# Kernel tuning notes

Hardware: AMD Instinct MI355X
Metric: run time of the kernel (lower is better)

The kernel has to match this reference:

```python
import jax, jax.numpy as jnp
import numpy as np

B, C, CI, H, W = 4, 256, 128, 64, 64  # batch, in_channels, inter_channels, spatial
EPS = 1e-5


def conv1x1(x, w, b):
    # x: [b,c,h,w], w: [o,c], b: [o] -> [b,o,h,w]
    return jnp.einsum('bchw,oc->bohw', x, w) + b[None, :, None, None]


def setup_inputs() -> dict:
    key = jax.random.key(0)
    ks = jax.random.split(key, 16)
    s_in = 1.0 / np.sqrt(C)
    s_mid = 1.0 / np.sqrt(CI)
    inp = {
        'feats_all': jax.random.normal(ks[0], (B, C, H, W), dtype=jnp.float32),
        'human_feats': jax.random.normal(ks[1], (B, C, H, W), dtype=jnp.float32),
        'g_w': jax.random.uniform(ks[2], (CI, C), jnp.float32, -s_in, s_in),
        'g_b': jax.random.uniform(ks[3], (CI,), jnp.float32, -s_in, s_in),
        'theta_w': jax.random.uniform(ks[4], (CI, C), jnp.float32, -s_in, s_in),
        'theta_b': jax.random.uniform(ks[5], (CI,), jnp.float32, -s_in, s_in),
        'phi_w': jax.random.uniform(ks[6], (CI, C), jnp.float32, -s_in, s_in),
        'phi_b': jax.random.uniform(ks[7], (CI,), jnp.float32, -s_in, s_in),
        'human_theta_w': jax.random.uniform(ks[8], (CI, C), jnp.float32, -s_in, s_in),
        'human_theta_b': jax.random.uniform(ks[9], (CI,), jnp.float32, -s_in, s_in),
        'human_phi_w': jax.random.uniform(ks[10], (CI, C), jnp.float32, -s_in, s_in),
        'human_phi_b': jax.random.uniform(ks[11], (CI,), jnp.float32, -s_in, s_in),
        'W_w': jax.random.uniform(ks[12], (C, CI), jnp.float32, -s_mid, s_mid),
        'W_b': jax.random.uniform(ks[13], (C,), jnp.float32, -s_mid, s_mid),
        'bn_gamma': jax.random.normal(ks[14], (C,), dtype=jnp.float32) * 0.1 + 1.0,
        'bn_beta': jax.random.normal(ks[15], (C,), dtype=jnp.float32) * 0.1,
        'bn_mean': jnp.zeros((C,), jnp.float32),
        'bn_var': jnp.ones((C,), jnp.float32),
    }
    return inp


def reference(feats_all, human_feats, g_w, g_b, theta_w, theta_b, phi_w, phi_b,
              human_theta_w, human_theta_b, human_phi_w, human_phi_b,
              W_w, W_b, bn_gamma, bn_beta, bn_mean, bn_var):
    b = feats_all.shape[0]
    n = H * W
    scale = CI ** -0.5

    # human attention map: softmax over keys of scaled QK^T
    hq = conv1x1(human_feats, human_theta_w, human_theta_b).reshape(b, CI, n)  # [b,ci,n]
    hk = conv1x1(human_feats, human_phi_w, human_phi_b).reshape(b, CI, n)
    human_map = jax.nn.softmax(scale * jnp.einsum('bcq,bck->bqk', hq, hk), axis=-1)

    # standard non-local map on feats_all
    th = conv1x1(feats_all, theta_w, theta_b).reshape(b, CI, n)
    ph = conv1x1(feats_all, phi_w, phi_b).reshape(b, CI, n)
    f = jax.nn.softmax(scale * jnp.einsum('bcq,bck->bqk', th, ph), axis=-1)

    g_x = conv1x1(feats_all, g_w, g_b).reshape(b, CI, n)  # [b,ci,n]

    attn = (human_map + f) * 0.5                          # [b,n,n]
    y = jnp.einsum('bqk,bck->bcq', attn, g_x)             # [b,ci,n]
    y = y.reshape(b, CI, H, W)

    wy = conv1x1(y, W_w, W_b)                             # [b,C,H,W]
    # BatchNorm2d (eval mode, running stats)
    inv = bn_gamma / jnp.sqrt(bn_var + EPS)
    out = (wy - bn_mean[None, :, None, None]) * inv[None, :, None, None] + bn_beta[None, :, None, None]
    return out
```

## Files before the change

### kernel.cpp

```cpp
#include <hip/hip_runtime.h>

#define DEVI __device__ __forceinline__

typedef float f32x4 __attribute__((ext_vector_type(4)));
typedef float f32x16 __attribute__((ext_vector_type(16)));
typedef unsigned int u32x4 __attribute__((ext_vector_type(4)));
typedef unsigned int u32x2 __attribute__((ext_vector_type(2)));
typedef __bf16 bf16x8 __attribute__((ext_vector_type(8)));

#define NB 4
#define CIN 256
#define CI_ 128
#define NN 4096
#define QSCALE 0.12752792233895158f

typedef unsigned short us;

DEVI us f2bf(float f) {
  unsigned int x = __float_as_uint(f);
  x += 0x7FFFu + ((x >> 16) & 1u);
  return (us)(x >> 16);
}

DEVI unsigned cvtpk(float lo, float hi) {
  unsigned r;
  asm("v_cvt_pk_bf16_f32 %0, %1, %2" : "=v"(r) : "v"(lo), "v"(hi));
  return r;
}

DEVI void plswap(unsigned& a, unsigned& b) {
  asm volatile("v_permlane32_swap_b32 %0, %1" : "+v"(a), "+v"(b));
}

DEVI float exp2fast(float x) {
#if __has_builtin(__builtin_amdgcn_exp2f)
  return __builtin_amdgcn_exp2f(x);
#else
  return exp2f(x);
#endif
}

DEVI f32x4 mfma16(u32x4 a, u32x4 b, f32x4 c) {
  return __builtin_amdgcn_mfma_f32_16x16x32_bf16(
      __builtin_bit_cast(bf16x8, a), __builtin_bit_cast(bf16x8, b), c, 0, 0, 0);
}

DEVI f32x16 mfma32(u32x4 a, u32x4 b, f32x16 c) {
  return __builtin_amdgcn_mfma_f32_32x32x16_bf16(
      __builtin_bit_cast(bf16x8, a), __builtin_bit_cast(bf16x8, b), c, 0, 0, 0);
}

DEVI void gload16(const void* g, void* l) {
  __builtin_amdgcn_global_load_lds(
      (const __attribute__((address_space(1))) void*)g,
      (__attribute__((address_space(3))) void*)l, 16, 0, 0);
}

DEVI void softpack(f32x16& a, float& ls, u32x4* pa) {
#pragma unroll
  for (int r = 0; r < 16; ++r) {
    float e = exp2fast(a[r]);
    ls += e;
    a[r] = e;
  }
  unsigned x0 = cvtpk(a[0], a[1]), z0 = cvtpk(a[2], a[3]);
  unsigned y0 = cvtpk(a[4], a[5]), t0 = cvtpk(a[6], a[7]);
  plswap(x0, y0);
  plswap(z0, t0);
  pa[0][0] = x0; pa[0][1] = z0; pa[0][2] = y0; pa[0][3] = t0;
  unsigned x1 = cvtpk(a[8], a[9]), z1 = cvtpk(a[10], a[11]);
  unsigned y1 = cvtpk(a[12], a[13]), t1 = cvtpk(a[14], a[15]);
  plswap(x1, y1);
  plswap(z1, t1);
  pa[1][0] = x1; pa[1][1] = z1; pa[1][2] = y1; pa[1][3] = t1;
}

__global__ __launch_bounds__(256) void wcvt_kernel(
    const float* __restrict__ hth_w, const float* __restrict__ hph_w,
    const float* __restrict__ th_w, const float* __restrict__ ph_w,
    const float* __restrict__ g_w, const float* __restrict__ Ww,
    us* __restrict__ wb) {
  const float* srcs[6] = {hth_w, hph_w, th_w, ph_w, g_w, Ww};
  const float* s = srcs[blockIdx.y];
  us* d = wb + blockIdx.y * 32768;
  int idx = (blockIdx.x * 256 + threadIdx.x) * 4;
  f32x4 v = *(const f32x4*)(s + idx);
  u32x2 o;
  o[0] = cvtpk(v[0], v[1]);
  o[1] = cvtpk(v[2], v[3]);
  *(u32x2*)(d + idx) = o;
}

__global__ __launch_bounds__(256) void proj_kernel(
    const float* __restrict__ feats, const float* __restrict__ human,
    const float* __restrict__ g_b, const float* __restrict__ th_b,
    const float* __restrict__ ph_b, const float* __restrict__ hth_b,
    const float* __restrict__ hph_b, const us* __restrict__ wb,
    us* __restrict__ hqT, us* __restrict__ hkT,
    us* __restrict__ thT, us* __restrict__ phT, us* __restrict__ gP) {
  __shared__ alignas(16) us xt[64 * 256];
  const int t = threadIdx.x;
  const int b = blockIdx.y;
  const int n0 = blockIdx.x * 64;
  const int grp = blockIdx.z;
  const int w = t >> 6, l = t & 63, g16 = l >> 4, l15 = l & 15;
  const int tg = t >> 4, tl = t & 15;

  const float* src = grp ? feats : human;
#pragma unroll
  for (int i = 0; i < 8; ++i) {
    int p = i * 16 + tg;
    const float* s0 = src + (size_t)(b * CIN + 2 * p) * NN + n0 + tl * 4;
    f32x4 v0 = *(const f32x4*)s0;
    f32x4 v1 = *(const f32x4*)(s0 + NN);
#pragma unroll
    for (int j = 0; j < 4; ++j) {
      int row = tl * 4 + j;
      *(unsigned*)((char*)xt + row * 512 + ((4 * p) ^ ((row & 15) << 4))) =
          cvtpk(v0[j], v1[j]);
    }
  }
  __syncthreads();

  const float* pb2[2] = {grp ? th_b : hth_b, grp ? ph_b : hph_b};
  us* pout2[2] = {grp ? thT : hqT, grp ? phT : hkT};
  const us* wb0 = wb + grp * 2 * 32768;

  u32x4 afrag[8];
  const int arow = w * 16 + l15;
#pragma unroll
  for (int s = 0; s < 8; ++s)
    afrag[s] = *(const u32x4*)((const char*)xt + arow * 512 +
                               (((s << 6) | (g16 << 4)) ^ (l15 << 4)));
  for (int p = 0; p < 2; ++p) {
    const us* wbp = wb0 + p * 32768;
    const float scl = (p == 0) ? QSCALE : 1.0f;
    for (int nt = 0; nt < 8; ++nt) {
      f32x4 acc = {0.f, 0.f, 0.f, 0.f};
#pragma unroll
      for (int s = 0; s < 8; ++s) {
        u32x4 bf = *(const u32x4*)(wbp + (nt * 16 + l15) * 256 + s * 32 + g16 * 8);
        acc = mfma16(afrag[s], bf, acc);
      }
      float bias = pb2[p][nt * 16 + l15];
#pragma unroll
      for (int r = 0; r < 4; ++r) {
        int nrow = n0 + w * 16 + g16 * 4 + r;
        pout2[p][((size_t)b * NN + nrow) * CI_ + nt * 16 + l15] =
            f2bf((acc[r] + bias) * scl);
      }
    }
  }

  if (grp) {
    const us* wbg = wb + 4 * 32768;
    u32x4 ag[2][8];
#pragma unroll
    for (int mt = 0; mt < 2; ++mt)
#pragma unroll
      for (int s = 0; s < 8; ++s)
        ag[mt][s] = *(const u32x4*)(wbg + (w * 32 + mt * 16 + l15) * 256 + s * 32 + g16 * 8);
    float gb[2][4];
#pragma unroll
    for (int mt = 0; mt < 2; ++mt)
#pragma unroll
      for (int r = 0; r < 4; ++r) gb[mt][r] = g_b[w * 32 + mt * 16 + g16 * 4 + r];
    for (int nt = 0; nt < 4; ++nt) {
      f32x4 acc0 = {0.f, 0.f, 0.f, 0.f}, acc1 = {0.f, 0.f, 0.f, 0.f};
#pragma unroll
      for (int s = 0; s < 8; ++s) {
        u32x4 bf = *(const u32x4*)((const char*)xt + (nt * 16 + l15) * 512 +
                                   ((s * 64 + g16 * 16) ^ (l15 << 4)));
        acc0 = mfma16(ag[0][s], bf, acc0);
        acc1 = mfma16(ag[1][s], bf, acc1);
      }
#pragma unroll
      for (int r = 0; r < 4; ++r) {
        int ci0 = w * 32 + g16 * 4 + r;
        gP[((size_t)b * CI_ + ci0) * NN + n0 + nt * 16 + l15] = f2bf(acc0[r] + gb[0][r]);
        gP[((size_t)b * CI_ + ci0 + 16) * NN + n0 + nt * 16 + l15] = f2bf(acc1[r] + gb[1][r]);
      }
    }
  }
}

__global__ __launch_bounds__(128, 2) void attn_kernel(
    const us* __restrict__ hqT, const us* __restrict__ hkT,
    const us* __restrict__ thT, const us* __restrict__ phT,
    const us* __restrict__ gP, us* __restrict__ PY, float* __restrict__ PL) {
  __shared__ alignas(16) us sK[2][32 * 128];
  __shared__ alignas(16) us sV[2][32 * 128];

  const int t = threadIdx.x, w = t >> 6, l = t & 63;
  const int l31 = l & 31, hi = l >> 5, l15 = l & 15;
  const int id = blockIdx.x;
  const int bp = id & 7, b = bp & 3, path = bp >> 2;
  const int r2 = id >> 3, h = r2 & 1, chunk = r2 >> 1;
  const int qw = chunk * 64 + w * 32, kb = h * 2048;
  const us* Qs = (path ? thT : hqT) + (size_t)b * NN * CI_;
  const char* Kb = (const char*)((path ? phT : hkT) + (size_t)b * NN * CI_);
  const char* Vb = (const char*)(gP + (size_t)b * CI_ * NN);

  u32x4 aQ[8];
#pragma unroll
  for (int s = 0; s < 8; ++s)
    aQ[s] = *(const u32x4*)(Qs + (size_t)(qw + l31) * CI_ + s * 16 + hi * 8);

  f32x16 Y[4];
#pragma unroll
  for (int ds = 0; ds < 4; ++ds) Y[ds] = 0.f;
  float lsum = 0.f;

  const int sr = l >> 4;

  auto stage = [&](int k0, int buf) {
#pragma unroll
    for (int i = 0; i < 4; ++i) {
      int row = w * 16 + i * 4 + sr;
      gload16(Kb + (size_t)(k0 + row) * 256 + (((l & 15) ^ (row & 15)) << 4),
              (char*)sK[buf] + (w * 16 + i * 4) * 256);
    }
#pragma unroll
    for (int i = 0; i < 4; ++i) {
      int R = w * 16 + i * 4 + sr;
      int lu = (l & 15) ^ (R & 15);
      int d = 4 * R + (lu >> 2);
      gload16(Vb + (size_t)d * 8192 + (size_t)k0 * 2 + (lu & 3) * 16,
              (char*)sV[buf] + (w * 16 + i * 4) * 256);
    }
  };

  stage(kb, 0);
  __syncthreads();

  for (int kt = 0; kt < 64; ++kt) {
    const int cur = kt & 1;
    if (kt < 63) stage(kb + (kt + 1) * 32, cur ^ 1);
    const char* kt_ = (const char*)sK[cur];
    const char* vt_ = (const char*)sV[cur];

    f32x16 a0 = 0.f;
    __builtin_amdgcn_s_setprio(1);
#pragma unroll
    for (int s = 0; s < 8; ++s) {
      u32x4 ak = *(const u32x4*)(kt_ + l31 * 256 + (((s * 2 + hi) ^ l15) << 4));
      a0 = mfma32(ak, aQ[s], a0);
    }
    __builtin_amdgcn_s_setprio(0);

    u32x4 pa[2];
    softpack(a0, lsum, pa);

    __builtin_amdgcn_s_setprio(1);
#pragma unroll
    for (int ds = 0; ds < 4; ++ds) {
      int R = ds * 8 + (l31 >> 2);
      const char* vb = vt_ + R * 256;
      int k_ = R & 15;
      u32x4 v0 = *(const u32x4*)(vb + ((((l31 & 3) * 4 + hi) ^ k_) << 4));
      u32x4 v1 = *(const u32x4*)(vb + ((((l31 & 3) * 4 + 2 + hi) ^ k_) << 4));
      Y[ds] = mfma32(pa[0], v0, Y[ds]);
      Y[ds] = mfma32(pa[1], v1, Y[ds]);
    }
    __builtin_amdgcn_s_setprio(0);
    __syncthreads();
  }

  lsum += __shfl_xor(lsum, 32);
  if (hi == 0) PL[(size_t)(h * 8 + bp) * NN + qw + l31] = lsum;

  float* buf = (float*)(w ? (us*)sV : (us*)sK);
#pragma unroll
  for (int ds = 0; ds < 4; ++ds) {
    int d = ds * 32 + l31;
#pragma unroll
    for (int m = 0; m < 4; ++m) {
      f32x4 v = {Y[ds][4 * m], Y[ds][4 * m + 1], Y[ds][4 * m + 2],
                 Y[ds][4 * m + 3]};
      *(f32x4*)((char*)buf + d * 128 + (((2 * m + hi) ^ (d & 7)) << 4)) = v;
    }
  }
  float yv[64];
#pragma unroll
  for (int j = 0; j < 64; ++j) {
    int d = hi * 64 + j;
    yv[j] = *(const float*)((char*)buf + d * 128 +
                            ((((l31 >> 2) ^ (d & 7)) << 4)) + (l31 & 3) * 4);
  }
  us* dst = PY + ((size_t)(h * 8 + bp) * NN + qw + l31) * CI_ + hi * 64;
#pragma unroll
  for (int o = 0; o < 8; ++o) {
    u32x4 pk;
#pragma unroll
    for (int e = 0; e < 4; ++e)
      pk[e] = cvtpk(yv[o * 8 + 2 * e], yv[o * 8 + 2 * e + 1]);
    *(u32x4*)(dst + o * 8) = pk;
  }
}

__global__ __launch_bounds__(256) void wout_kernel(
    const us* __restrict__ PY, const float* __restrict__ PL,
    const us* __restrict__ wb, const float* __restrict__ Wb,
    const float* __restrict__ gamma, const float* __restrict__ beta,
    const float* __restrict__ mean, const float* __restrict__ var,
    float* __restrict__ out) {
  __shared__ alignas(16) us sY[64 * 128];
  const int t = threadIdx.x, w = t >> 6, l = t & 63, g16 = l >> 4, l15 = l & 15;
  const int n0 = blockIdx.x * 64;
  const int b = blockIdx.y;

  {
    const int row = t >> 2, cg = t & 3;
    const int n = n0 + row;
    float acc[32];
#pragma unroll
    for (int e = 0; e < 32; ++e) acc[e] = 0.f;
#pragma unroll
    for (int p = 0; p < 2; ++p) {
      int bpi = p * 4 + b;
      float sc = 0.5f / (PL[(size_t)bpi * NN + n] + PL[(size_t)(8 + bpi) * NN + n]);
#pragma unroll
      for (int hh = 0; hh < 2; ++hh) {
        const us* src = PY + (size_t)(hh * 8 + bpi) * (NN * CI_) +
                        (size_t)n * CI_ + cg * 32;
#pragma unroll
        for (int j = 0; j < 4; ++j) {
          u32x4 v = *(const u32x4*)(src + j * 8);
#pragma unroll
          for (int e = 0; e < 4; ++e) {
            unsigned u = v[e];
            acc[j * 8 + 2 * e] += __uint_as_float(u << 16) * sc;
            acc[j * 8 + 2 * e + 1] += __uint_as_float(u & 0xFFFF0000u) * sc;
          }
        }
      }
    }
#pragma unroll
    for (int j = 0; j < 4; ++j) {
      u32x4 o;
#pragma unroll
      for (int e = 0; e < 4; ++e)
        o[e] = cvtpk(acc[j * 8 + 2 * e], acc[j * 8 + 2 * e + 1]);
      *(u32x4*)((char*)sY + row * 256 + ((cg * 64 + j * 16) ^ ((row & 7) << 4))) = o;
    }
  }
  __syncthreads();

  const us* wbw = wb + 5 * 32768;
  for (int ob4 = 0; ob4 < 4; ++ob4) {
    const int ob = ob4 * 64;
    u32x4 aW[4];
    const int orow = ob + w * 16 + l15;
#pragma unroll
    for (int s = 0; s < 4; ++s)
      aW[s] = *(const u32x4*)(wbw + orow * 128 + s * 32 + g16 * 8);
    float wbias[4], inv_[4], mu[4], bt[4];
#pragma unroll
    for (int r = 0; r < 4; ++r) {
      int o = ob + w * 16 + g16 * 4 + r;
      wbias[r] = Wb[o];
      inv_[r] = gamma[o] * rsqrtf(var[o] + 1e-5f);
      mu[r] = mean[o];
      bt[r] = beta[o];
    }

    for (int nt = 0; nt < 4; ++nt) {
      f32x4 acc = {0.f, 0.f, 0.f, 0.f};
#pragma unroll
      for (int s = 0; s < 4; ++s) {
        u32x4 bf = *(const u32x4*)((const char*)sY + (nt * 16 + l15) * 256 +
                                   (((s << 6) | (g16 << 4)) ^ ((l15 & 7) << 4)));
        acc = mfma16(aW[s], bf, acc);
      }
#pragma unroll
      for (int r = 0; r < 4; ++r) {
        int o = ob + w * 16 + g16 * 4 + r;
        out[((size_t)b * CIN + o) * NN + n0 + nt * 16 + l15] =
            (acc[r] + wbias[r] - mu[r]) * inv_[r] + bt[r];
      }
    }
  }
}

extern "C" void kernel_launch(void* const* d_in, const int* in_sizes, int n_in,
                              void* d_out, int out_size, void* d_ws, size_t ws_size,
                              hipStream_t stream) {
  const float* feats = (const float*)d_in[0];
  const float* human = (const float*)d_in[1];
  const float* g_w = (const float*)d_in[2];
  const float* g_b = (const float*)d_in[3];
  const float* th_w = (const float*)d_in[4];
  const float* th_b = (const float*)d_in[5];
  const float* ph_w = (const float*)d_in[6];
  const float* ph_b = (const float*)d_in[7];
  const float* hth_w = (const float*)d_in[8];
  const float* hth_b = (const float*)d_in[9];
  const float* hph_w = (const float*)d_in[10];
  const float* hph_b = (const float*)d_in[11];
  const float* Ww = (const float*)d_in[12];
  const float* Wb = (const float*)d_in[13];
  const float* gamma = (const float*)d_in[14];
  const float* beta = (const float*)d_in[15];
  const float* mean = (const float*)d_in[16];
  const float* var = (const float*)d_in[17];

  us* ws = (us*)d_ws;
  const size_t SZ = (size_t)NB * NN * CI_;
  us* hqT = ws;
  us* hkT = ws + SZ;
  us* thT = ws + 2 * SZ;
  us* phT = ws + 3 * SZ;
  us* gP = ws + 4 * SZ;
  us* PY = ws + 5 * SZ;
  float* PL = (float*)(ws + 5 * SZ + 8388608);
  us* wb = ws + 5 * SZ + 8388608 + 131072;

  wcvt_kernel<<<dim3(32, 6), 256, 0, stream>>>(hth_w, hph_w, th_w, ph_w, g_w, Ww, wb);
  proj_kernel<<<dim3(64, 4, 2), 256, 0, stream>>>(feats, human, g_b, th_b, ph_b,
                                                  hth_b, hph_b, wb, hqT, hkT,
                                                  thT, phT, gP);
  attn_kernel<<<1024, 128, 0, stream>>>(hqT, hkT, thT, phT, gP, PY, PL);
  wout_kernel<<<dim3(64, 4), 256, 0, stream>>>(PY, PL, wb, Wb, gamma, beta,
                                               mean, var, (float*)d_out);
}
```

Baseline: 136.3 us.

## Widen attention blocks to 4 waves, 64 queries each, split keys four ways

The attention kernel now runs 256-thread blocks where each wave handles two 32-query tiles. Each staged K/V tile in shared memory is therefore reused across 256 queries instead of 64. Keys are split into four partitions instead of two, so the output kernel reduces four partial Y and row-sum buffers, and the workspace grows to hold them. The LDS transpose epilogue is replaced with direct scalar bf16 stores to PY, which are uncoalesced. The larger partial buffers also raise register pressure and memory traffic.

```diff
diff --git a/kernel.cpp b/kernel.cpp
--- a/kernel.cpp
+++ b/kernel.cpp
@@ -184,7 +184,7 @@
   }
 }
 
-__global__ __launch_bounds__(128, 2) void attn_kernel(
+__global__ __launch_bounds__(256, 2) void attn_kernel(
     const us* __restrict__ hqT, const us* __restrict__ hkT,
     const us* __restrict__ thT, const us* __restrict__ phT,
     const us* __restrict__ gP, us* __restrict__ PY, float* __restrict__ PL) {
@@ -195,61 +195,66 @@
   const int l31 = l & 31, hi = l >> 5, l15 = l & 15;
   const int id = blockIdx.x;
   const int bp = id & 7, b = bp & 3, path = bp >> 2;
-  const int r2 = id >> 3, h = r2 & 1, chunk = r2 >> 1;
-  const int qw = chunk * 64 + w * 32, kb = h * 2048;
+  const int r2 = id >> 3, h = r2 & 3, chunk = r2 >> 2;
+  const int qw = chunk * 256 + w * 64, kb = h * 1024;
   const us* Qs = (path ? thT : hqT) + (size_t)b * NN * CI_;
   const char* Kb = (const char*)((path ? phT : hkT) + (size_t)b * NN * CI_);
   const char* Vb = (const char*)(gP + (size_t)b * CI_ * NN);
 
-  u32x4 aQ[8];
-#pragma unroll
-  for (int s = 0; s < 8; ++s)
-    aQ[s] = *(const u32x4*)(Qs + (size_t)(qw + l31) * CI_ + s * 16 + hi * 8);
-
-  f32x16 Y[4];
-#pragma unroll
-  for (int ds = 0; ds < 4; ++ds) Y[ds] = 0.f;
-  float lsum = 0.f;
-
-  const int sr = l >> 4;
+  u32x4 aQ[2][8];
+#pragma unroll
+  for (int qs = 0; qs < 2; ++qs)
+#pragma unroll
+    for (int s = 0; s < 8; ++s)
+      aQ[qs][s] = *(const u32x4*)(Qs + (size_t)(qw + qs * 32 + l31) * CI_ +
+                                  s * 16 + hi * 8);
+
+  f32x16 Y[2][4];
+#pragma unroll
+  for (int qs = 0; qs < 2; ++qs)
+#pragma unroll
+    for (int ds = 0; ds < 4; ++ds) Y[qs][ds] = 0.f;
+  float lsum[2] = {0.f, 0.f};
 
   auto stage = [&](int k0, int buf) {
 #pragma unroll
-    for (int i = 0; i < 4; ++i) {
-      int row = w * 16 + i * 4 + sr;
+    for (int i = 0; i < 2; ++i) {
+      int row = i * 16 + w * 4 + (l >> 4);
       gload16(Kb + (size_t)(k0 + row) * 256 + (((l & 15) ^ (row & 15)) << 4),
-              (char*)sK[buf] + (w * 16 + i * 4) * 256);
-    }
-#pragma unroll
-    for (int i = 0; i < 4; ++i) {
-      int R = w * 16 + i * 4 + sr;
+              (char*)sK[buf] + (i * 16 + w * 4) * 256);
+    }
+#pragma unroll
+    for (int i = 0; i < 2; ++i) {
+      int R = i * 16 + w * 4 + (l >> 4);
       int lu = (l & 15) ^ (R & 15);
       int d = 4 * R + (lu >> 2);
       gload16(Vb + (size_t)d * 8192 + (size_t)k0 * 2 + (lu & 3) * 16,
-              (char*)sV[buf] + (w * 16 + i * 4) * 256);
+              (char*)sV[buf] + (i * 16 + w * 4) * 256);
     }
   };
 
   stage(kb, 0);
   __syncthreads();
 
-  for (int kt = 0; kt < 64; ++kt) {
+  for (int kt = 0; kt < 32; ++kt) {
     const int cur = kt & 1;
-    if (kt < 63) stage(kb + (kt + 1) * 32, cur ^ 1);
+    if (kt < 31) stage(kb + (kt + 1) * 32, cur ^ 1);
     const char* kt_ = (const char*)sK[cur];
     const char* vt_ = (const char*)sV[cur];
 
-    f32x16 a0 = 0.f;
+    f32x16 a0 = 0.f, a1 = 0.f;
     __builtin_amdgcn_s_setprio(1);
 #pragma unroll
     for (int s = 0; s < 8; ++s) {
       u32x4 ak = *(const u32x4*)(kt_ + l31 * 256 + (((s * 2 + hi) ^ l15) << 4));
-      a0 = mfma32(ak, aQ[s], a0);
+      a0 = mfma32(ak, aQ[0][s], a0);
+      a1 = mfma32(ak, aQ[1][s], a1);
     }
     __builtin_amdgcn_s_setprio(0);
 
-    u32x4 pa[2];
-    softpack(a0, lsum, pa);
+    u32x4 pa0[2], pa1[2];
+    softpack(a0, lsum[0], pa0);
+    softpack(a1, lsum[1], pa1);
 
     __builtin_amdgcn_s_setprio(1);
 #pragma unroll
@@ -259,43 +264,34 @@
       int k_ = R & 15;
       u32x4 v0 = *(const u32x4*)(vb + ((((l31 & 3) * 4 + hi) ^ k_) << 4));
       u32x4 v1 = *(const u32x4*)(vb + ((((l31 & 3) * 4 + 2 + hi) ^ k_) << 4));
-      Y[ds] = mfma32(pa[0], v0, Y[ds]);
-      Y[ds] = mfma32(pa[1], v1, Y[ds]);
+      Y[0][ds] = mfma32(pa0[0], v0, Y[0][ds]);
+      Y[0][ds] = mfma32(pa0[1], v1, Y[0][ds]);
+      Y[1][ds] = mfma32(pa1[0], v0, Y[1][ds]);
+      Y[1][ds] = mfma32(pa1[1], v1, Y[1][ds]);
     }
     __builtin_amdgcn_s_setprio(0);
     __syncthreads();
   }
 
-  lsum += __shfl_xor(lsum, 32);
-  if (hi == 0) PL[(size_t)(h * 8 + bp) * NN + qw + l31] = lsum;
-
-  float* buf = (float*)(w ? (us*)sV : (us*)sK);
-#pragma unroll
-  for (int ds = 0; ds < 4; ++ds) {
-    int d = ds * 32 + l31;
-#pragma unroll
-    for (int m = 0; m < 4; ++m) {
-      f32x4 v = {Y[ds][4 * m], Y[ds][4 * m + 1], Y[ds][4 * m + 2],
-                 Y[ds][4 * m + 3]};
-      *(f32x4*)((char*)buf + d * 128 + (((2 * m + hi) ^ (d & 7)) << 4)) = v;
-    }
-  }
-  float yv[64];
-#pragma unroll
-  for (int j = 0; j < 64; ++j) {
-    int d = hi * 64 + j;
-    yv[j] = *(const float*)((char*)buf + d * 128 +
-                            ((((l31 >> 2) ^ (d & 7)) << 4)) + (l31 & 3) * 4);
-  }
-  us* dst = PY + ((size_t)(h * 8 + bp) * NN + qw + l31) * CI_ + hi * 64;
-#pragma unroll
-  for (int o = 0; o < 8; ++o) {
-    u32x4 pk;
-#pragma unroll
-    for (int e = 0; e < 4; ++e)
-      pk[e] = cvtpk(yv[o * 8 + 2 * e], yv[o * 8 + 2 * e + 1]);
-    *(u32x4*)(dst + o * 8) = pk;
-  }
+  lsum[0] += __shfl_xor(lsum[0], 32);
+  lsum[1] += __shfl_xor(lsum[1], 32);
+  const size_t pb_ = (size_t)(h * 8 + bp) * NN;
+  if (hi == 0) {
+    PL[pb_ + qw + l31] = lsum[0];
+    PL[pb_ + qw + 32 + l31] = lsum[1];
+  }
+#pragma unroll
+  for (int qs = 0; qs < 2; ++qs)
+#pragma unroll
+    for (int ds = 0; ds < 4; ++ds)
+#pragma unroll
+      for (int m = 0; m < 4; ++m)
+#pragma unroll
+        for (int e = 0; e < 4; ++e) {
+          int q = qw + qs * 32 + 8 * m + 4 * hi + e;
+          PY[(pb_ + q) * CI_ + ds * 32 + l31] =
+              (us)cvtpk(Y[qs][ds][4 * m + e], 0.f);
+        }
 }
 
 __global__ __launch_bounds__(256) void wout_kernel(
@@ -318,9 +314,12 @@
 #pragma unroll
     for (int p = 0; p < 2; ++p) {
       int bpi = p * 4 + b;
-      float sc = 0.5f / (PL[(size_t)bpi * NN + n] + PL[(size_t)(8 + bpi) * NN + n]);
-#pragma unroll
-      for (int hh = 0; hh < 2; ++hh) {
+      float den = 0.f;
+#pragma unroll
+      for (int hh = 0; hh < 4; ++hh) den += PL[(size_t)(hh * 8 + bpi) * NN + n];
+      float sc = 0.5f / den;
+#pragma unroll
+      for (int hh = 0; hh < 4; ++hh) {
         const us* src = PY + (size_t)(hh * 8 + bpi) * (NN * CI_) +
                         (size_t)n * CI_ + cg * 32;
 #pragma unroll
@@ -412,14 +411,14 @@
   us* phT = ws + 3 * SZ;
   us* gP = ws + 4 * SZ;
   us* PY = ws + 5 * SZ;
-  float* PL = (float*)(ws + 5 * SZ + 8388608);
-  us* wb = ws + 5 * SZ + 8388608 + 131072;
+  float* PL = (float*)(ws + 5 * SZ + 16777216);
+  us* wb = ws + 5 * SZ + 16777216 + 262144;
 
   wcvt_kernel<<<dim3(32, 6), 256, 0, stream>>>(hth_w, hph_w, th_w, ph_w, g_w, Ww, wb);
   proj_kernel<<<dim3(64, 4, 2), 256, 0, stream>>>(feats, human, g_b, th_b, ph_b,
                                                   hth_b, hph_b, wb, hqT, hkT,
                                                   thT, phT, gP);
-  attn_kernel<<<1024, 128, 0, stream>>>(hqT, hkT, thT, phT, gP, PY, PL);
+  attn_kernel<<<512, 256, 0, stream>>>(hqT, hkT, thT, phT, gP, PY, PL);
   wout_kernel<<<dim3(64, 4), 256, 0, stream>>>(PY, PL, wb, Wb, gamma, beta,
                                                mean, var, (float*)d_out);
 }
```

New measurement: 148.2 us. 8.8% more time.
